# Performance work log

Measured on AMD Instinct MI355X. Metric: run time of the kernel, lower is better.

## Reference

```python
import jax, jax.numpy as jnp
import numpy as np

D_MODEL = 1024
N_HEADS = 16
HEAD_DIM = D_MODEL // N_HEADS


def setup_inputs() -> dict:
    key = jax.random.key(0)
    ks = jax.random.split(key, 9)
    B, T, S, D = 4, 2048, 512, D_MODEL
    sc = 1.0 / np.sqrt(D)
    return {
        "x": jax.random.normal(ks[0], (B, T, D), dtype=jnp.float32),
        "context": jax.random.normal(ks[1], (B, S, D), dtype=jnp.float32),
        "context_mask": jnp.ones((B, S), dtype=bool),
        "Wq": jax.random.normal(ks[2], (D, D), dtype=jnp.float32) * sc,
        "bq": jnp.zeros((D,), dtype=jnp.float32),
        "Wkv": jax.random.normal(ks[3], (D, 2 * D), dtype=jnp.float32) * sc,
        "bkv": jnp.zeros((2 * D,), dtype=jnp.float32),
        "Wp": jax.random.normal(ks[4], (D, D), dtype=jnp.float32) * sc,
        "bp": jnp.zeros((D,), dtype=jnp.float32),
    }


def reference(x, context, context_mask, Wq, bq, Wkv, bkv, Wp, bp):
    B, T, D = x.shape
    S = context.shape[1]
    H, Hd = N_HEADS, HEAD_DIM
    # projections
    q = (x @ Wq + bq).reshape(B, T, H, Hd).transpose(0, 2, 1, 3)          # [B,H,T,Hd]
    kv = (context @ Wkv + bkv).reshape(B, S, 2, H, Hd)
    k = kv[:, :, 0].transpose(0, 2, 1, 3)                                  # [B,H,S,Hd]
    v = kv[:, :, 1].transpose(0, 2, 1, 3)                                  # [B,H,S,Hd]
    # scaled dot-product attention with context mask
    scores = jnp.einsum("bhtd,bhsd->bhts", q, k) / np.sqrt(Hd)            # [B,H,T,S]
    neg_inf = jnp.finfo(scores.dtype).min
    scores = jnp.where(context_mask[:, None, None, :], scores, neg_inf)
    attn = jax.nn.softmax(scores, axis=-1)
    # dropout is identity in eval mode (p applied only in training)
    out = jnp.einsum("bhts,bhsd->bthd", attn, v).reshape(B, T, D)
    return out @ Wp + bp
```

## Files before the change

kernel.cpp:

```cpp
#include <hip/hip_runtime.h>

typedef __bf16 bf16x8 __attribute__((ext_vector_type(8)));
typedef float  f32x4  __attribute__((ext_vector_type(4)));

#define MFMA(a, b, c) __builtin_amdgcn_mfma_f32_16x16x32_bf16((a), (b), (c), 0, 0, 0)

#define GLL(g, l) __builtin_amdgcn_global_load_lds(                                  \
    (const __attribute__((address_space(1))) void*)(g),                              \
    (__attribute__((address_space(3))) void*)(l), 16, 0, 0)

#define BB 4
#define TT 2048
#define SS 512
#define DM 1024
#define NH 16
#define HD 64

__device__ __forceinline__ unsigned short f2bh(float f) {
    __bf16 h = (__bf16)f;
    union { __bf16 h; unsigned short u; } v; v.h = h;
    return v.u;
}

__device__ __forceinline__ void tcast_tile(const float* __restrict__ in,
                                           unsigned short* __restrict__ out,
                                           int K, int N, int n0, int k0,
                                           float (*tile)[33], int tid) {
    int tx = tid & 31, ty = tid >> 5;
#pragma unroll
    for (int r = 0; r < 32; r += 8)
        tile[ty + r][tx] = in[(k0 + ty + r) * N + n0 + tx];
    __syncthreads();
    int r2 = tid >> 3, cg = (tid & 7) * 4;
    ushort4 o;
    o.x = f2bh(tile[cg + 0][r2]);
    o.y = f2bh(tile[cg + 1][r2]);
    o.z = f2bh(tile[cg + 2][r2]);
    o.w = f2bh(tile[cg + 3][r2]);
    *(ushort4*)&out[(n0 + r2) * K + k0 + cg] = o;
}

__global__ __launch_bounds__(256)
void prep(const float4* __restrict__ x, const float4* __restrict__ ctx,
          const unsigned int* __restrict__ mw,
          const float* __restrict__ Wq, const float* __restrict__ Wkv,
          const float* __restrict__ Wp,
          ushort4* __restrict__ Xbf, ushort4* __restrict__ Cbf,
          unsigned short* __restrict__ WqT, unsigned short* __restrict__ WkvT,
          unsigned short* __restrict__ WpT, float* __restrict__ mbias) {
    __shared__ float tile[32][33];
    __shared__ int flags[2];
    const int bid = blockIdx.x, tid = threadIdx.x;
    if (bid < 8192) {
        int i = bid * 256 + tid;
        float4 v = x[i];
        ushort4 o; o.x = f2bh(v.x); o.y = f2bh(v.y); o.z = f2bh(v.z); o.w = f2bh(v.w);
        Xbf[i] = o;
    } else if (bid < 10240) {
        int i = (bid - 8192) * 256 + tid;
        float4 v = ctx[i];
        ushort4 o; o.x = f2bh(v.x); o.y = f2bh(v.y); o.z = f2bh(v.z); o.w = f2bh(v.w);
        Cbf[i] = o;
    } else if (bid < 11264) {
        int loc = bid - 10240;
        tcast_tile(Wq, WqT, DM, DM, (loc & 31) * 32, (loc >> 5) * 32, tile, tid);
    } else if (bid < 13312) {
        int loc = bid - 11264;
        tcast_tile(Wkv, WkvT, DM, 2 * DM, (loc & 63) * 32, (loc >> 6) * 32, tile, tid);
    } else if (bid < 14336) {
        int loc = bid - 13312;
        tcast_tile(Wp, WpT, DM, DM, (loc & 31) * 32, (loc >> 5) * 32, tile, tid);
    } else {
        if (tid == 0) { flags[0] = 1; flags[1] = 1; }
        __syncthreads();
        int okI = 1, okF = 1;
        for (int i = tid; i < 512; i += 256) {
            unsigned int w = mw[i];
            if (w > 1u) okI = 0;
            if (w != 0u && w != 0x3f800000u) okF = 0;
        }
        if (!okI) atomicAnd(&flags[0], 0);
        if (!okF) atomicAnd(&flags[1], 0);
        __syncthreads();
        bool wordLayout = (flags[0] != 0) || (flags[1] != 0);
        const unsigned char* mb = (const unsigned char*)mw;
        for (int s = tid; s < BB * SS; s += 256) {
            bool on = wordLayout ? (mw[s] != 0u) : (mb[s] != 0);
            mbias[s] = on ? 0.0f : -1e38f;
        }
    }
}

__device__ __forceinline__ void gemm_core(
    const unsigned short* __restrict__ A, const unsigned short* __restrict__ Bt,
    int K, int m0, int n0, unsigned short* As, unsigned short* Bs,
    f32x4 (*acc)[4]) {
    const int tid = threadIdx.x;
    const int l = tid & 63;
    const int quad = l >> 4, col = l & 15;
    const int w = tid >> 6;
    const int wm = (w & 1) * 64, wn = (w >> 1) * 64;
    const int arow = tid >> 3;
    const int apiece = (tid & 7) ^ (arow & 7);
    const unsigned short* Ab = A + (size_t)(m0 + arow) * K + apiece * 8;
    const unsigned short* Bb = Bt + (size_t)(n0 + arow) * K + apiece * 8;

    for (int k0 = 0; k0 < K; k0 += 64) {
        __syncthreads();
#pragma unroll
        for (int g = 0; g < 4; ++g)
            GLL(Ab + k0 + g * 32 * K, &As[g * 2048 + tid * 8]);
#pragma unroll
        for (int g = 0; g < 4; ++g)
            GLL(Bb + k0 + g * 32 * K, &Bs[g * 2048 + tid * 8]);
        __syncthreads();
#pragma unroll
        for (int k32 = 0; k32 < 2; ++k32) {
            bf16x8 af[4], bfr[4];
#pragma unroll
            for (int i = 0; i < 4; i++) {
                int rr = wm + i * 16 + col;
                af[i] = *(const bf16x8*)&As[rr * 64 + (((k32 * 4 + quad) ^ (rr & 7)) * 8)];
            }
#pragma unroll
            for (int j = 0; j < 4; j++) {
                int rr = wn + j * 16 + col;
                bfr[j] = *(const bf16x8*)&Bs[rr * 64 + (((k32 * 4 + quad) ^ (rr & 7)) * 8)];
            }
#pragma unroll
            for (int i = 0; i < 4; i++)
#pragma unroll
                for (int j = 0; j < 4; j++) acc[i][j] = MFMA(af[i], bfr[j], acc[i][j]);
        }
    }
}

__global__ __launch_bounds__(256, 3)
void gemm_qkv(const unsigned short* __restrict__ Xbf, const unsigned short* __restrict__ WqT,
              const float* __restrict__ bq, unsigned short* __restrict__ Qb,
              const unsigned short* __restrict__ Cbf, const unsigned short* __restrict__ WkvT,
              const float* __restrict__ bkv, unsigned short* __restrict__ Kb,
              unsigned short* __restrict__ Vtb) {
    __shared__ __align__(16) unsigned short As[128 * 64];
    __shared__ __align__(16) unsigned short Bs[128 * 64];
    const int tid = threadIdx.x;
    const int l = tid & 63;
    const int quad = l >> 4, col = l & 15;
    const int w = tid >> 6;
    const int wm = (w & 1) * 64, wn = (w >> 1) * 64;
    const int bid = blockIdx.x;

    const f32x4 zero = {0.f, 0.f, 0.f, 0.f};
    f32x4 acc[4][4];
#pragma unroll
    for (int i = 0; i < 4; i++)
#pragma unroll
        for (int j = 0; j < 4; j++) acc[i][j] = zero;

    if (bid < 512) {
        const int xg = bid & 7, t = bid >> 3;
        const int m0 = (xg + 8 * (t & 7)) * 128;
        const int n0 = (t >> 3) * 128;
        gemm_core(Xbf, WqT, DM, m0, n0, As, Bs, acc);
        const float QS = 0.125f * 1.4426950408889634f;
#pragma unroll
        for (int i = 0; i < 4; i++) {
#pragma unroll
            for (int j = 0; j < 4; j++) {
                int n = n0 + wn + j * 16 + col;
                int mb = m0 + wm + i * 16 + quad * 4;
                float bv = bq[n];
#pragma unroll
                for (int ii = 0; ii < 4; ii++)
                    Qb[(mb + ii) * DM + n] = f2bh((acc[i][j][ii] + bv) * QS);
            }
        }
    } else {
        const int loc = bid - 512;
        const int xg = loc & 7, t = loc >> 3;
        const int m0 = (xg + 8 * (t & 1)) * 128;
        const int n0 = (t >> 1) * 128;
        gemm_core(Cbf, WkvT, DM, m0, n0, As, Bs, acc);
#pragma unroll
        for (int i = 0; i < 4; i++) {
#pragma unroll
            for (int j = 0; j < 4; j++) {
                int n = n0 + wn + j * 16 + col;
                int mb = m0 + wm + i * 16 + quad * 4;
                float bv = bkv[n];
                if (n < 1024) {
                    int h = n >> 6, d = n & 63;
#pragma unroll
                    for (int ii = 0; ii < 4; ii++) {
                        int m = mb + ii; int b = m >> 9, s = m & 511;
                        Kb[(((b * NH + h) * SS) + s) * HD + d] = f2bh(acc[i][j][ii] + bv);
                    }
                } else {
                    int q = n - 1024; int h = q >> 6, d = q & 63;
#pragma unroll
                    for (int ii = 0; ii < 4; ii++) {
                        int m = mb + ii; int b = m >> 9, s = m & 511;
                        Vtb[(((b * NH + h) * HD) + d) * SS + s] = f2bh(acc[i][j][ii] + bv);
                    }
                }
            }
        }
    }
}

__global__ __launch_bounds__(256, 3)
void gemm_out(const unsigned short* __restrict__ Ob, const unsigned short* __restrict__ WpT,
              const float* __restrict__ bp, float* __restrict__ out) {
    __shared__ __align__(16) unsigned short As[128 * 64];
    __shared__ __align__(16) unsigned short Bs[128 * 64];
    const int tid = threadIdx.x;
    const int l = tid & 63;
    const int quad = l >> 4, col = l & 15;
    const int w = tid >> 6;
    const int wm = (w & 1) * 64, wn = (w >> 1) * 64;
    const int bid = blockIdx.x;
    const int xg = bid & 7, t = bid >> 3;
    const int m0 = (xg + 8 * (t & 7)) * 128;
    const int n0 = (t >> 3) * 128;

    const f32x4 zero = {0.f, 0.f, 0.f, 0.f};
    f32x4 acc[4][4];
#pragma unroll
    for (int i = 0; i < 4; i++)
#pragma unroll
        for (int j = 0; j < 4; j++) acc[i][j] = zero;

    gemm_core(Ob, WpT, DM, m0, n0, As, Bs, acc);

#pragma unroll
    for (int i = 0; i < 4; i++) {
#pragma unroll
        for (int j = 0; j < 4; j++) {
            int n = n0 + wn + j * 16 + col;
            int mb = m0 + wm + i * 16 + quad * 4;
            float bv = bp[n];
#pragma unroll
            for (int ii = 0; ii < 4; ii++)
                out[(mb + ii) * DM + n] = acc[i][j][ii] + bv;
        }
    }
}

__global__ __launch_bounds__(512, 4)
void flash_attn(const unsigned short* __restrict__ Q, const unsigned short* __restrict__ Kb,
                const unsigned short* __restrict__ Vt, const float* __restrict__ mbias,
                unsigned short* __restrict__ O) {
    const int bid = blockIdx.x;
    const int xg = bid & 7, tq = bid >> 3;
    const int tb = tq & 7;
    const int bh = xg + 8 * (tq >> 3);
    const int b = bh >> 4;
    const int tid = threadIdx.x;
    const int w = tid >> 6, l = tid & 63;
    const int quad = l >> 4, col = l & 15;

    __shared__ __align__(16) unsigned short Ks[2][64 * 64];
    __shared__ __align__(16) unsigned short Vs[2][64 * 64];
    __shared__ __align__(16) unsigned short Pb[8][2][32 * 32];
    __shared__ float biasS[SS];

    const unsigned short* Kh = Kb + bh * SS * HD;
    const unsigned short* Vh = Vt + bh * HD * SS;

    float bval = mbias[b * SS + tid];
    biasS[tid] = bval;
    const int allon = __syncthreads_and(bval == 0.0f);

    const int rowbase = b * TT + tb * 256 + w * 32;
    bf16x8 qf[2][2];
#pragma unroll
    for (int rg = 0; rg < 2; rg++) {
        const unsigned short* qrow = Q + (rowbase + rg * 16 + col) * DM + (bh & 15) * HD;
        qf[rg][0] = *(const bf16x8*)(qrow + quad * 8);
        qf[rg][1] = *(const bf16x8*)(qrow + 32 + quad * 8);
    }

    const int sr = tid >> 3, sp = tid & 7;
    const int spk = ((sp ^ (sr & 7)) * 8);
    const int kgo = sr * HD + spk;
    const int vgo = sr * SS + spk;

    GLL(Kh + kgo, &Ks[0][tid * 8]);
    GLL(Vh + vgo, &Vs[0][tid * 8]);

    const f32x4 zero = {0.f, 0.f, 0.f, 0.f};
    f32x4 o[2][4];
#pragma unroll
    for (int rg = 0; rg < 2; rg++)
#pragma unroll
        for (int j = 0; j < 4; j++) o[rg][j] = zero;
    f32x4 lacc[2] = {zero, zero};
    bf16x8 onesb;
#pragma unroll
    for (int z = 0; z < 8; z++) onesb[z] = (__bf16)1.0f;

    for (int it = 0; it < SS / 64; ++it) {
        const int s0 = it * 64;
        const int buf = it & 1;
        __syncthreads();
        if (it + 1 < SS / 64) {
            GLL(Kh + (s0 + 64) * HD + kgo, &Ks[buf ^ 1][tid * 8]);
            GLL(Vh + (s0 + 64) + vgo, &Vs[buf ^ 1][tid * 8]);
        }

#pragma unroll
        for (int h2 = 0; h2 < 2; ++h2) {
            f32x4 sc[2][2];
#pragma unroll
            for (int jj = 0; jj < 2; ++jj) {
                int row = (2 * h2 + jj) * 16 + col;
                bf16x8 k0 = *(const bf16x8*)&Ks[buf][row * 64 + ((quad ^ (row & 7)) * 8)];
                bf16x8 k1 = *(const bf16x8*)&Ks[buf][row * 64 + (((4 + quad) ^ (row & 7)) * 8)];
                __builtin_amdgcn_s_setprio(1);
#pragma unroll
                for (int rg = 0; rg < 2; rg++) {
                    f32x4 tt = MFMA(qf[rg][0], k0, zero);
                    sc[rg][jj] = MFMA(qf[rg][1], k1, tt);
                }
                __builtin_amdgcn_s_setprio(0);
            }
            if (allon) {
#pragma unroll
                for (int rg = 0; rg < 2; rg++)
#pragma unroll
                    for (int jj = 0; jj < 2; jj++)
#pragma unroll
                        for (int i = 0; i < 4; i++) {
                            float p = exp2f(sc[rg][jj][i]);
                            int row = rg * 16 + quad * 4 + i;
                            int s = jj * 16 + col;
                            int pc = (s >> 3) ^ ((row >> 1) & 3);
                            Pb[w][h2][(row << 5) + (pc << 3) + (s & 7)] = f2bh(p);
                        }
            } else {
#pragma unroll
                for (int rg = 0; rg < 2; rg++)
#pragma unroll
                    for (int jj = 0; jj < 2; jj++) {
                        float bb = biasS[s0 + (2 * h2 + jj) * 16 + col];
#pragma unroll
                        for (int i = 0; i < 4; i++) {
                            float p = exp2f(sc[rg][jj][i] + bb);
                            int row = rg * 16 + quad * 4 + i;
                            int s = jj * 16 + col;
                            int pc = (s >> 3) ^ ((row >> 1) & 3);
                            Pb[w][h2][(row << 5) + (pc << 3) + (s & 7)] = f2bh(p);
                        }
                    }
            }
        }

#pragma unroll
        for (int h2 = 0; h2 < 2; ++h2) {
            bf16x8 pf[2];
#pragma unroll
            for (int rg = 0; rg < 2; rg++) {
                int prow = rg * 16 + col;
                int pp = quad ^ ((col >> 1) & 3);
                pf[rg] = *(const bf16x8*)&Pb[w][h2][(prow << 5) + (pp << 3)];
            }
            __builtin_amdgcn_s_setprio(1);
#pragma unroll
            for (int rg = 0; rg < 2; rg++) lacc[rg] = MFMA(pf[rg], onesb, lacc[rg]);
#pragma unroll
            for (int j2 = 0; j2 < 4; j2++) {
                int row = j2 * 16 + col;
                bf16x8 vf = *(const bf16x8*)&Vs[buf][row * 64 + (((h2 * 4 + quad) ^ (row & 7)) * 8)];
#pragma unroll
                for (int rg = 0; rg < 2; rg++)
                    o[rg][j2] = MFMA(pf[rg], vf, o[rg][j2]);
            }
            __builtin_amdgcn_s_setprio(0);
        }
    }

#pragma unroll
    for (int rg = 0; rg < 2; rg++) {
#pragma unroll
        for (int i = 0; i < 4; i++) {
            float inv = 1.0f / lacc[rg][i];
            unsigned short* orow = O + (rowbase + rg * 16 + quad * 4 + i) * DM
                                     + (bh & 15) * HD + col;
#pragma unroll
            for (int j2 = 0; j2 < 4; j2++)
                orow[j2 * 16] = f2bh(o[rg][j2][i] * inv);
        }
    }
}

extern "C" void kernel_launch(void* const* d_in, const int* in_sizes, int n_in,
                              void* d_out, int out_size, void* d_ws, size_t ws_size,
                              hipStream_t stream) {
    const float* x    = (const float*)d_in[0];
    const float* ctx  = (const float*)d_in[1];
    const void*  cmsk = d_in[2];
    const float* Wq   = (const float*)d_in[3];
    const float* bq   = (const float*)d_in[4];
    const float* Wkv  = (const float*)d_in[5];
    const float* bkv  = (const float*)d_in[6];
    const float* Wp   = (const float*)d_in[7];
    const float* bp   = (const float*)d_in[8];
    float* out = (float*)d_out;

    char* ws = (char*)d_ws;
    size_t off = 0;
    auto alloc = [&](size_t bytes) -> void* {
        void* p = ws + off;
        off += (bytes + 255) & ~(size_t)255;
        return p;
    };
    const size_t NX = (size_t)BB * TT * DM;
    const size_t NC = (size_t)BB * SS * DM;
    unsigned short* Xbf  = (unsigned short*)alloc(NX * 2);
    unsigned short* Cbf  = (unsigned short*)alloc(NC * 2);
    unsigned short* WqT  = (unsigned short*)alloc((size_t)DM * DM * 2);
    unsigned short* WkvT = (unsigned short*)alloc((size_t)DM * 2 * DM * 2);
    unsigned short* WpT  = (unsigned short*)alloc((size_t)DM * DM * 2);
    unsigned short* Qb   = (unsigned short*)alloc(NX * 2);
    unsigned short* Kbf  = (unsigned short*)alloc(NC * 2);
    unsigned short* Vtb  = (unsigned short*)alloc(NC * 2);
    unsigned short* Ob   = (unsigned short*)alloc(NX * 2);
    float* mbias         = (float*)alloc((size_t)BB * SS * 4);

    prep<<<14337, 256, 0, stream>>>((const float4*)x, (const float4*)ctx,
                                    (const unsigned int*)cmsk, Wq, Wkv, Wp,
                                    (ushort4*)Xbf, (ushort4*)Cbf,
                                    WqT, WkvT, WpT, mbias);

    gemm_qkv<<<768, 256, 0, stream>>>(Xbf, WqT, bq, Qb, Cbf, WkvT, bkv, Kbf, Vtb);

    flash_attn<<<BB * NH * (TT / 256), 512, 0, stream>>>(Qb, Kbf, Vtb, mbias, Ob);

    gemm_out<<<512, 256, 0, stream>>>(Ob, WpT, bp, out);
}
```

Measured before the change: 208.9 us.

## Switch flash attention to 32x32 MFMA with register-resident P via permlane swaps

Rewrites the attention inner loop to use 32x32x16 bf16 MFMAs. Scores are computed transposed (K as the A operand) so each lane holds a column of P that can be packed into the PV MFMA operand with permlane32_swap instead of a round trip through LDS. The P shared buffer and the ones-vector MFMA for row sums are removed; row sums are now accumulated in scalar registers and redistributed with ds_bpermute at the end. The intent is to cut LDS traffic and MFMA instruction count, at the cost of more register pressure and fragile lane-mapping logic.

```diff
diff --git a/kernel.cpp b/kernel.cpp
--- a/kernel.cpp
+++ b/kernel.cpp
@@ -2,8 +2,11 @@
 
 typedef __bf16 bf16x8 __attribute__((ext_vector_type(8)));
 typedef float  f32x4  __attribute__((ext_vector_type(4)));
-
-#define MFMA(a, b, c) __builtin_amdgcn_mfma_f32_16x16x32_bf16((a), (b), (c), 0, 0, 0)
+typedef float  f32x16 __attribute__((ext_vector_type(16)));
+typedef unsigned int u32x2 __attribute__((ext_vector_type(2)));
+
+#define MFMA(a, b, c)   __builtin_amdgcn_mfma_f32_16x16x32_bf16((a), (b), (c), 0, 0, 0)
+#define MFMA32(a, b, c) __builtin_amdgcn_mfma_f32_32x32x16_bf16((a), (b), (c), 0, 0, 0)
 
 #define GLL(g, l) __builtin_amdgcn_global_load_lds(                                  \
     (const __attribute__((address_space(1))) void*)(g),                              \
@@ -20,6 +23,15 @@
     __bf16 h = (__bf16)f;
     union { __bf16 h; unsigned short u; } v; v.h = h;
     return v.u;
+}
+
+__device__ __forceinline__ unsigned int pk2(float a, float b) {
+    return (unsigned int)f2bh(a) | ((unsigned int)f2bh(b) << 16);
+}
+
+__device__ __forceinline__ void pl32swap(unsigned int& a, unsigned int& b) {
+    u32x2 r = __builtin_amdgcn_permlane32_swap(a, b, false, false);
+    a = r[0]; b = r[1];
 }
 
 __device__ __forceinline__ void tcast_tile(const float* __restrict__ in,
@@ -257,11 +269,10 @@
     const int b = bh >> 4;
     const int tid = threadIdx.x;
     const int w = tid >> 6, l = tid & 63;
-    const int quad = l >> 4, col = l & 15;
+    const int lq = l & 31, hi = l >> 5;
 
     __shared__ __align__(16) unsigned short Ks[2][64 * 64];
     __shared__ __align__(16) unsigned short Vs[2][64 * 64];
-    __shared__ __align__(16) unsigned short Pb[8][2][32 * 32];
     __shared__ float biasS[SS];
 
     const unsigned short* Kh = Kb + bh * SS * HD;
@@ -272,13 +283,13 @@
     const int allon = __syncthreads_and(bval == 0.0f);
 
     const int rowbase = b * TT + tb * 256 + w * 32;
-    bf16x8 qf[2][2];
-#pragma unroll
-    for (int rg = 0; rg < 2; rg++) {
-        const unsigned short* qrow = Q + (rowbase + rg * 16 + col) * DM + (bh & 15) * HD;
-        qf[rg][0] = *(const bf16x8*)(qrow + quad * 8);
-        qf[rg][1] = *(const bf16x8*)(qrow + 32 + quad * 8);
-    }
+    const int hd0 = (bh & 15) * HD;
+
+    const unsigned short* qrow = Q + (size_t)(rowbase + lq) * DM + hd0;
+    bf16x8 qf[4];
+#pragma unroll
+    for (int ch = 0; ch < 4; ++ch)
+        qf[ch] = *(const bf16x8*)(qrow + ch * 16 + hi * 8);
 
     const int sr = tid >> 3, sp = tid & 7;
     const int spk = ((sp ^ (sr & 7)) * 8);
@@ -288,16 +299,10 @@
     GLL(Kh + kgo, &Ks[0][tid * 8]);
     GLL(Vh + vgo, &Vs[0][tid * 8]);
 
-    const f32x4 zero = {0.f, 0.f, 0.f, 0.f};
-    f32x4 o[2][4];
-#pragma unroll
-    for (int rg = 0; rg < 2; rg++)
-#pragma unroll
-        for (int j = 0; j < 4; j++) o[rg][j] = zero;
-    f32x4 lacc[2] = {zero, zero};
-    bf16x8 onesb;
-#pragma unroll
-    for (int z = 0; z < 8; z++) onesb[z] = (__bf16)1.0f;
+    const f32x16 zero16 = {0.f,0.f,0.f,0.f,0.f,0.f,0.f,0.f,
+                           0.f,0.f,0.f,0.f,0.f,0.f,0.f,0.f};
+    f32x16 oacc0 = zero16, oacc1 = zero16;
+    float lsum = 0.f;
 
     for (int it = 0; it < SS / 64; ++it) {
         const int s0 = it * 64;
@@ -308,88 +313,67 @@
             GLL(Vh + (s0 + 64) + vgo, &Vs[buf ^ 1][tid * 8]);
         }
 
-#pragma unroll
-        for (int h2 = 0; h2 < 2; ++h2) {
-            f32x4 sc[2][2];
-#pragma unroll
-            for (int jj = 0; jj < 2; ++jj) {
-                int row = (2 * h2 + jj) * 16 + col;
-                bf16x8 k0 = *(const bf16x8*)&Ks[buf][row * 64 + ((quad ^ (row & 7)) * 8)];
-                bf16x8 k1 = *(const bf16x8*)&Ks[buf][row * 64 + (((4 + quad) ^ (row & 7)) * 8)];
-                __builtin_amdgcn_s_setprio(1);
-#pragma unroll
-                for (int rg = 0; rg < 2; rg++) {
-                    f32x4 tt = MFMA(qf[rg][0], k0, zero);
-                    sc[rg][jj] = MFMA(qf[rg][1], k1, tt);
-                }
-                __builtin_amdgcn_s_setprio(0);
+        f32x16 cs0 = zero16, cs1 = zero16;
+        __builtin_amdgcn_s_setprio(1);
+#pragma unroll
+        for (int ch = 0; ch < 4; ++ch) {
+            const int p0 = ((2 * ch + hi) ^ (lq & 7)) * 8;
+            bf16x8 k0 = *(const bf16x8*)&Ks[buf][lq * 64 + p0];
+            bf16x8 k1 = *(const bf16x8*)&Ks[buf][(lq + 32) * 64 + p0];
+            cs0 = MFMA32(k0, qf[ch], cs0);
+            cs1 = MFMA32(k1, qf[ch], cs1);
+        }
+        __builtin_amdgcn_s_setprio(0);
+
+        bf16x8 pfrag[4];
+#pragma unroll
+        for (int sg = 0; sg < 2; ++sg) {
+            float pr[16];
+#pragma unroll
+            for (int r = 0; r < 16; ++r) {
+                float sc = (sg == 0) ? cs0[r] : cs1[r];
+                if (!allon)
+                    sc += biasS[s0 + 32 * sg + ((r & 3) + 8 * (r >> 2) + 4 * hi)];
+                pr[r] = exp2f(sc);
+                lsum += pr[r];
             }
-            if (allon) {
-#pragma unroll
-                for (int rg = 0; rg < 2; rg++)
-#pragma unroll
-                    for (int jj = 0; jj < 2; jj++)
-#pragma unroll
-                        for (int i = 0; i < 4; i++) {
-                            float p = exp2f(sc[rg][jj][i]);
-                            int row = rg * 16 + quad * 4 + i;
-                            int s = jj * 16 + col;
-                            int pc = (s >> 3) ^ ((row >> 1) & 3);
-                            Pb[w][h2][(row << 5) + (pc << 3) + (s & 7)] = f2bh(p);
-                        }
-            } else {
-#pragma unroll
-                for (int rg = 0; rg < 2; rg++)
-#pragma unroll
-                    for (int jj = 0; jj < 2; jj++) {
-                        float bb = biasS[s0 + (2 * h2 + jj) * 16 + col];
-#pragma unroll
-                        for (int i = 0; i < 4; i++) {
-                            float p = exp2f(sc[rg][jj][i] + bb);
-                            int row = rg * 16 + quad * 4 + i;
-                            int s = jj * 16 + col;
-                            int pc = (s >> 3) ^ ((row >> 1) & 3);
-                            Pb[w][h2][(row << 5) + (pc << 3) + (s & 7)] = f2bh(p);
-                        }
-                    }
-            }
-        }
-
-#pragma unroll
-        for (int h2 = 0; h2 < 2; ++h2) {
-            bf16x8 pf[2];
-#pragma unroll
-            for (int rg = 0; rg < 2; rg++) {
-                int prow = rg * 16 + col;
-                int pp = quad ^ ((col >> 1) & 3);
-                pf[rg] = *(const bf16x8*)&Pb[w][h2][(prow << 5) + (pp << 3)];
-            }
-            __builtin_amdgcn_s_setprio(1);
-#pragma unroll
-            for (int rg = 0; rg < 2; rg++) lacc[rg] = MFMA(pf[rg], onesb, lacc[rg]);
-#pragma unroll
-            for (int j2 = 0; j2 < 4; j2++) {
-                int row = j2 * 16 + col;
-                bf16x8 vf = *(const bf16x8*)&Vs[buf][row * 64 + (((h2 * 4 + quad) ^ (row & 7)) * 8)];
-#pragma unroll
-                for (int rg = 0; rg < 2; rg++)
-                    o[rg][j2] = MFMA(pf[rg], vf, o[rg][j2]);
-            }
-            __builtin_amdgcn_s_setprio(0);
-        }
-    }
-
-#pragma unroll
-    for (int rg = 0; rg < 2; rg++) {
-#pragma unroll
-        for (int i = 0; i < 4; i++) {
-            float inv = 1.0f / lacc[rg][i];
-            unsigned short* orow = O + (rowbase + rg * 16 + quad * 4 + i) * DM
-                                     + (bh & 15) * HD + col;
-#pragma unroll
-            for (int j2 = 0; j2 < 4; j2++)
-                orow[j2 * 16] = f2bh(o[rg][j2][i] * inv);
-        }
+            unsigned int wd0 = pk2(pr[0], pr[1]),  wd1 = pk2(pr[2], pr[3]);
+            unsigned int wd2 = pk2(pr[4], pr[5]),  wd3 = pk2(pr[6], pr[7]);
+            unsigned int wd4 = pk2(pr[8], pr[9]),  wd5 = pk2(pr[10], pr[11]);
+            unsigned int wd6 = pk2(pr[12], pr[13]), wd7 = pk2(pr[14], pr[15]);
+            pl32swap(wd0, wd2); pl32swap(wd1, wd3);
+            pl32swap(wd4, wd6); pl32swap(wd5, wd7);
+            union { unsigned int u[4]; bf16x8 v; } f0, f1;
+            f0.u[0] = wd0; f0.u[1] = wd1; f0.u[2] = wd2; f0.u[3] = wd3;
+            f1.u[0] = wd4; f1.u[1] = wd5; f1.u[2] = wd6; f1.u[3] = wd7;
+            pfrag[2 * sg + 0] = f0.v;
+            pfrag[2 * sg + 1] = f1.v;
+        }
+
+        __builtin_amdgcn_s_setprio(1);
+#pragma unroll
+        for (int win = 0; win < 4; ++win) {
+            const int pv0 = ((2 * win + hi) ^ (lq & 7)) * 8;
+            bf16x8 v0 = *(const bf16x8*)&Vs[buf][lq * 64 + pv0];
+            bf16x8 v1 = *(const bf16x8*)&Vs[buf][(lq + 32) * 64 + pv0];
+            oacc0 = MFMA32(pfrag[win], v0, oacc0);
+            oacc1 = MFMA32(pfrag[win], v1, oacc1);
+        }
+        __builtin_amdgcn_s_setprio(0);
+    }
+
+    lsum += __shfl_xor(lsum, 32);
+    float inv = 1.0f / lsum;
+    union { float f; int i; } cv; cv.f = inv;
+#pragma unroll
+    for (int r = 0; r < 16; ++r) {
+        const int qloc = (r & 3) + 8 * (r >> 2) + 4 * hi;
+        union { int i; float f; } rv;
+        rv.i = __builtin_amdgcn_ds_bpermute(4 * qloc, cv.i);
+        const float iq = rv.f;
+        unsigned short* orow = O + (size_t)(rowbase + qloc) * DM + hd0 + lq;
+        orow[0]  = f2bh(oacc0[r] * iq);
+        orow[32] = f2bh(oacc1[r] * iq);
     }
 }
 
```

Result: faster. 200.4 us (-4.1%).
